# Optimization experiments

Measured on AMD Instinct MI355X. Metric: run time of the kernel, lower is better.

Reference implementation:

```python
import jax, jax.numpy as jnp
import numpy as np

B, C, H, W = 4, 256, 64, 64
G, K, P = 4, 7, 3          # groups, kernel size, padding
RED = 32                   # out_channels // reduce_ratio
BN_EPS = 1e-5


def setup_inputs() -> dict:
    key = jax.random.key(0)
    ks = jax.random.split(key, 3)
    x = jax.random.normal(ks[0], (B, C, H, W), dtype=jnp.float32)
    w_reduce = jax.random.normal(ks[1], (RED, C), dtype=jnp.float32) * (1.0 / np.sqrt(C))
    bn_gamma = jnp.ones((RED,), dtype=jnp.float32)
    bn_beta = jnp.zeros((RED,), dtype=jnp.float32)
    w_span = jax.random.normal(ks[2], (K * K * G, RED), dtype=jnp.float32) * (1.0 / np.sqrt(RED))
    b_span = jnp.zeros((K * K * G,), dtype=jnp.float32)
    return {"x": x, "w_reduce": w_reduce, "bn_gamma": bn_gamma,
            "bn_beta": bn_beta, "w_span": w_span, "b_span": b_span}


def _involution(x, w_reduce, bn_gamma, bn_beta, w_span, b_span):
    # ---- dynamic kernel generation (stride=1 so AvgPool is identity) ----
    red = jnp.einsum('oc,bchw->bohw', w_reduce, x)                 # [B,RED,H,W]
    # BatchNorm2d forward with batch statistics (training-mode math)
    mean = red.mean(axis=(0, 2, 3), keepdims=True)
    var = red.var(axis=(0, 2, 3), keepdims=True)
    red_n = (red - mean) * jax.lax.rsqrt(var + BN_EPS)
    act = jax.nn.relu(red_n * bn_gamma[None, :, None, None] + bn_beta[None, :, None, None])
    ker = jnp.einsum('oc,bchw->bohw', w_span, act) + b_span[None, :, None, None]
    ker = ker.reshape(B, G, K * K, H, W)                           # [B,G,KK,H,W]

    # ---- unfold: K*K shifted views of the padded input ----
    xp = jnp.pad(x, ((0, 0), (0, 0), (P, P), (P, P)))
    patches = jnp.stack([xp[:, :, i:i + H, j:j + W]
                         for i in range(K) for j in range(K)], axis=2)  # [B,C,KK,H,W]
    patches = patches.reshape(B, G, C // G, K * K, H, W)

    # ---- per-pixel weighted neighborhood sum ----
    out = jnp.einsum('bgkhw,bgckhw->bgchw', ker, patches)
    return out.reshape(B, C, H, W)


def reference(x, w_reduce, bn_gamma, bn_beta, w_span, b_span):
    return _involution(x, w_reduce, bn_gamma, bn_beta, w_span, b_span)
```

## Files before the change

### kernel.cpp

```cpp
#include <hip/hip_runtime.h>

#define B_ 4
#define C_ 256
#define H_ 64
#define W_ 64
#define HW_ 4096
#define K_ 7
#define P_ 3
#define KK_ 49
#define KKG_ 196
#define RED_ 32
#define NSTAT_ 16384.0f
#define BN_EPS_ 1e-5f
#define OCH_ 28

#define CPB_ 8
#define TH_ 16
#define TRS_ 22
#define TRW_ 76

__global__ __launch_bounds__(256) void k_reduce(const float* __restrict__ x,
                                               const float* __restrict__ wr,
                                               float4* __restrict__ part,
                                               float* __restrict__ gstats) {
    const int tid = threadIdx.x;
    const int og  = blockIdx.y;
    const int bz  = blockIdx.z;
    if (blockIdx.x == 0 && og == 0 && bz == 0 && tid < 64) gstats[tid] = 0.0f;

    const int p2 = blockIdx.x * 256 + tid;
    const int b  = p2 >> 11;
    const int hw = (p2 & 2047) << 1;
    const float* xp = x + ((size_t)(b * C_ + bz * 64)) * HW_ + hw;
    const float* wp = wr + (og * 8) * C_ + bz * 64;

    float a[8][2];
#pragma unroll
    for (int oi = 0; oi < 8; ++oi) { a[oi][0] = 0.f; a[oi][1] = 0.f; }
#pragma unroll 8
    for (int cc = 0; cc < 64; ++cc) {
        const float2 v = *(const float2*)(xp + (size_t)cc * HW_);
#pragma unroll
        for (int oi = 0; oi < 8; ++oi) {
            const float wv = wp[oi * C_ + cc];
            a[oi][0] = fmaf(wv, v.x, a[oi][0]);
            a[oi][1] = fmaf(wv, v.y, a[oi][1]);
        }
    }
    const int slot = bz * 4 + og;
    float4* pp0 = part + (((size_t)(slot * 2 + 0)) << 14) + (p2 << 1);
    float4* pp1 = part + (((size_t)(slot * 2 + 1)) << 14) + (p2 << 1);
    pp0[0] = make_float4(a[0][0], a[1][0], a[2][0], a[3][0]);
    pp0[1] = make_float4(a[0][1], a[1][1], a[2][1], a[3][1]);
    pp1[0] = make_float4(a[4][0], a[5][0], a[6][0], a[7][0]);
    pp1[1] = make_float4(a[4][1], a[5][1], a[6][1], a[7][1]);
}

__global__ __launch_bounds__(256) void k_comb(const float4* __restrict__ part,
                                              float4* __restrict__ red,
                                              float* __restrict__ gsum,
                                              float* __restrict__ gsq) {
    __shared__ float lsum[4][8];
    const int tid  = threadIdx.x;
    const int lane = tid & 63;
    const int wv   = tid >> 6;
    const int oq   = blockIdx.y;
    const int og   = oq >> 1;
    const int half = oq & 1;
    const int p    = blockIdx.x * 256 + tid;

    float4 s = make_float4(0.f, 0.f, 0.f, 0.f);
#pragma unroll
    for (int bz = 0; bz < 4; ++bz) {
        const float4 v = part[(((size_t)((bz * 4 + og) * 2 + half)) << 14) + p];
        s.x += v.x; s.y += v.y; s.z += v.z; s.w += v.w;
    }
    red[((size_t)oq << 14) + p] = s;

    float s0 = s.x, s1 = s.y, s2 = s.z, s3 = s.w;
    float q0 = s.x*s.x, q1 = s.y*s.y, q2 = s.z*s.z, q3 = s.w*s.w;
#pragma unroll
    for (int off = 32; off > 0; off >>= 1) {
        s0 += __shfl_down(s0, off);  q0 += __shfl_down(q0, off);
        s1 += __shfl_down(s1, off);  q1 += __shfl_down(q1, off);
        s2 += __shfl_down(s2, off);  q2 += __shfl_down(q2, off);
        s3 += __shfl_down(s3, off);  q3 += __shfl_down(q3, off);
    }
    if (lane == 0) {
        lsum[wv][0] = s0; lsum[wv][1] = s1; lsum[wv][2] = s2; lsum[wv][3] = s3;
        lsum[wv][4] = q0; lsum[wv][5] = q1; lsum[wv][6] = q2; lsum[wv][7] = q3;
    }
    __syncthreads();
    if (tid < 8) {
        const float v = lsum[0][tid] + lsum[1][tid] + lsum[2][tid] + lsum[3][tid];
        float* dst = (tid < 4) ? &gsum[oq * 4 + tid] : &gsq[oq * 4 + (tid - 4)];
        atomicAdd(dst, v);
    }
}

__global__ __launch_bounds__(256) void k_span(const float4* __restrict__ red,
                                              const float* __restrict__ wspan,
                                              const float* __restrict__ bspan,
                                              const float* __restrict__ gsum,
                                              const float* __restrict__ gsq,
                                              const float* __restrict__ gamma,
                                              const float* __restrict__ beta,
                                              float* __restrict__ ker) {
    __shared__ float sc_l[RED_], sh_l[RED_];
    const int tid   = threadIdx.x;
    const int chunk = blockIdx.y;
    const int obase = chunk * OCH_;
    if (tid < RED_) {
        const float m   = gsum[tid] * (1.0f / NSTAT_);
        const float var = gsq[tid] * (1.0f / NSTAT_) - m * m;
        const float inv = rsqrtf(var + BN_EPS_);
        const float sc  = gamma[tid] * inv;
        sc_l[tid] = sc;
        sh_l[tid] = beta[tid] - m * sc;
    }
    __syncthreads();

    const int p  = blockIdx.x * 256 + tid;
    const int b  = p >> 12;
    const int hw = p & 4095;

    float act[RED_];
#pragma unroll
    for (int og = 0; og < 8; ++og) {
        const float4 v = red[((size_t)og << 14) + p];
        act[4*og+0] = v.x; act[4*og+1] = v.y; act[4*og+2] = v.z; act[4*og+3] = v.w;
    }
#pragma unroll
    for (int o = 0; o < RED_; ++o)
        act[o] = fmaxf(fmaf(act[o], sc_l[o], sh_l[o]), 0.0f);

    float* kp = ker + ((size_t)b * KKG_ + obase) * HW_ + hw;
    const float* wp = wspan + (size_t)obase * RED_;
#pragma unroll 4
    for (int o = 0; o < OCH_; ++o) {
        float s = bspan[obase + o];
#pragma unroll
        for (int c = 0; c < RED_; ++c)
            s = fmaf(wp[o * RED_ + c], act[c], s);
        kp[(size_t)o * HW_] = s;
    }
}

__global__ __launch_bounds__(256) void k_inv(const float* __restrict__ x,
                                             const float* __restrict__ ker,
                                             float* __restrict__ out) {
    __shared__ float tile[CPB_][TRS_][TRW_];
    const int tid = threadIdx.x;
    const int wg  = tid & 7;
    const int hq  = (tid >> 3) & 15;
    const int cq  = tid >> 7;
    const int bx  = blockIdx.x;
    const int ht  = bx & 3;
    const int cblk = (bx >> 2) & 31;
    const int b   = bx >> 7;
    const int h0  = ht << 4;
    const int c0  = cblk << 3;
    const int g   = c0 >> 6;
    const int w0  = wg << 3;
    const int h   = h0 + hq;

    const float4 fz = make_float4(0.f, 0.f, 0.f, 0.f);
#pragma unroll
    for (int it = 0; it < 11; ++it) {
        const int i   = it * 256 + tid;
        const int ci  = i / (TRS_ * 16);
        const int rem = i - ci * (TRS_ * 16);
        const int r   = rem >> 4;
        const int seg = rem & 15;
        const int hh  = h0 + r - P_;
        float4 v = fz;
        if (hh >= 0 && hh < H_)
            v = *(const float4*)(x + (((size_t)(b * C_ + c0 + ci)) << 12) + (hh << 6) + (seg << 2));
        *(float4*)&tile[ci][r][4 + (seg << 2)] = v;
    }
    for (int i = tid; i < CPB_ * TRS_ * 2; i += 256) {
        const int ci  = i / (TRS_ * 2);
        const int rem = i - ci * (TRS_ * 2);
        const int r   = rem >> 1;
        *(float4*)&tile[ci][r][(rem & 1) ? 68 : 0] = fz;
    }
    __syncthreads();

    const int cA = cq << 2;
    const float* kp = ker + (((size_t)b * KKG_ + g * KK_) << 12) + (h << 6) + w0;

    float acc[4][8];
#pragma unroll
    for (int c = 0; c < 4; ++c)
#pragma unroll
        for (int dw = 0; dw < 8; ++dw) acc[c][dw] = 0.f;

#pragma unroll
    for (int i = 0; i < K_; ++i) {
        const int r = hq + i;
        float win[4][16];
#pragma unroll
        for (int c = 0; c < 4; ++c) {
            const float* t = &tile[cA + c][r][w0];
#pragma unroll
            for (int s = 0; s < 4; ++s) {
                const float4 v = *(const float4*)(t + (s << 2));
                win[c][4*s+0]=v.x; win[c][4*s+1]=v.y; win[c][4*s+2]=v.z; win[c][4*s+3]=v.w;
            }
        }
#pragma unroll
        for (int j = 0; j < K_; ++j) {
            const float* kpp = kp + ((size_t)(i * K_ + j) << 12);
            const float4 k0 = *(const float4*)kpp;
            const float4 k1 = *(const float4*)(kpp + 4);
            const float kv[8] = {k0.x, k0.y, k0.z, k0.w, k1.x, k1.y, k1.z, k1.w};
#pragma unroll
            for (int c = 0; c < 4; ++c)
#pragma unroll
                for (int dw = 0; dw < 8; ++dw)
                    acc[c][dw] = fmaf(kv[dw], win[c][dw + j + 1], acc[c][dw]);
        }
    }

#pragma unroll
    for (int c = 0; c < 4; ++c) {
        float* o = out + (((size_t)(b * C_ + c0 + cA + c)) << 12) + (h << 6) + w0;
        *(float4*)(o)     = make_float4(acc[c][0], acc[c][1], acc[c][2], acc[c][3]);
        *(float4*)(o + 4) = make_float4(acc[c][4], acc[c][5], acc[c][6], acc[c][7]);
    }
}

extern "C" void kernel_launch(void* const* d_in, const int* in_sizes, int n_in,
                              void* d_out, int out_size, void* d_ws, size_t ws_size,
                              hipStream_t stream) {
    const float* x     = (const float*)d_in[0];
    const float* wr    = (const float*)d_in[1];
    const float* gamma = (const float*)d_in[2];
    const float* beta  = (const float*)d_in[3];
    const float* wspan = (const float*)d_in[4];
    const float* bspan = (const float*)d_in[5];
    float* out = (float*)d_out;
    float* ws  = (float*)d_ws;

    float*  redf  = ws;
    float*  gsum  = ws + 524288;
    float*  gsq   = gsum + 32;
    float*  ker   = ws + 524416;
    float*  partf = ws + 524416 + 3211264;
    float4* red   = (float4*)redf;
    float4* part  = (float4*)partf;

    hipLaunchKernelGGL(k_reduce, dim3(32, 4, 4), dim3(256), 0, stream, x, wr, part, gsum);
    hipLaunchKernelGGL(k_comb,   dim3(64, 8),    dim3(256), 0, stream, part, red, gsum, gsq);
    hipLaunchKernelGGL(k_span,   dim3(64, 7),    dim3(256), 0, stream, red, wspan, bspan, gsum, gsq, gamma, beta, ker);
    hipLaunchKernelGGL(k_inv,    dim3(512),      dim3(256), 0, stream, x, ker, out);
}
```

Before: 58.72 us.

## Compute all 32 reduce channels per thread and regroup involution blocks by group

k_reduce now has each thread produce all 32 reduced outputs for one pixel, instead of 8 outputs for two pixels split across four output-group blocks. Each x value is therefore loaded once per channel slice rather than four times, cutting redundant global reads. The cost is more accumulator registers and fewer blocks (256 instead of 512), which may lower occupancy. k_inv block indexing is also remapped so that consecutive blocks share a group's kernel weights, which should improve cache locality for the ker reads.

```diff
diff --git a/kernel.cpp b/kernel.cpp
--- a/kernel.cpp
+++ b/kernel.cpp
@@ -24,36 +24,31 @@
                                                float4* __restrict__ part,
                                                float* __restrict__ gstats) {
     const int tid = threadIdx.x;
-    const int og  = blockIdx.y;
-    const int bz  = blockIdx.z;
-    if (blockIdx.x == 0 && og == 0 && bz == 0 && tid < 64) gstats[tid] = 0.0f;
-
-    const int p2 = blockIdx.x * 256 + tid;
-    const int b  = p2 >> 11;
-    const int hw = (p2 & 2047) << 1;
+    const int bz  = blockIdx.y;
+    if (blockIdx.x == 0 && bz == 0 && tid < 64) gstats[tid] = 0.0f;
+
+    const int p  = blockIdx.x * 256 + tid;
+    const int b  = p >> 12;
+    const int hw = p & 4095;
     const float* xp = x + ((size_t)(b * C_ + bz * 64)) * HW_ + hw;
-    const float* wp = wr + (og * 8) * C_ + bz * 64;
-
-    float a[8][2];
-#pragma unroll
-    for (int oi = 0; oi < 8; ++oi) { a[oi][0] = 0.f; a[oi][1] = 0.f; }
+    const float* wp = wr + bz * 64;
+
+    float a[32];
+#pragma unroll
+    for (int o = 0; o < 32; ++o) a[o] = 0.0f;
+
 #pragma unroll 8
     for (int cc = 0; cc < 64; ++cc) {
-        const float2 v = *(const float2*)(xp + (size_t)cc * HW_);
-#pragma unroll
-        for (int oi = 0; oi < 8; ++oi) {
-            const float wv = wp[oi * C_ + cc];
-            a[oi][0] = fmaf(wv, v.x, a[oi][0]);
-            a[oi][1] = fmaf(wv, v.y, a[oi][1]);
-        }
-    }
-    const int slot = bz * 4 + og;
-    float4* pp0 = part + (((size_t)(slot * 2 + 0)) << 14) + (p2 << 1);
-    float4* pp1 = part + (((size_t)(slot * 2 + 1)) << 14) + (p2 << 1);
-    pp0[0] = make_float4(a[0][0], a[1][0], a[2][0], a[3][0]);
-    pp0[1] = make_float4(a[0][1], a[1][1], a[2][1], a[3][1]);
-    pp1[0] = make_float4(a[4][0], a[5][0], a[6][0], a[7][0]);
-    pp1[1] = make_float4(a[4][1], a[5][1], a[6][1], a[7][1]);
+        const float v = xp[(size_t)cc * HW_];
+#pragma unroll
+        for (int o = 0; o < 32; ++o)
+            a[o] = fmaf(wp[o * C_ + cc], v, a[o]);
+    }
+
+#pragma unroll
+    for (int q = 0; q < 8; ++q)
+        part[(((size_t)(bz * 8 + q)) << 14) + p] =
+            make_float4(a[4*q], a[4*q+1], a[4*q+2], a[4*q+3]);
 }
 
 __global__ __launch_bounds__(256) void k_comb(const float4* __restrict__ part,
@@ -65,14 +60,12 @@
     const int lane = tid & 63;
     const int wv   = tid >> 6;
     const int oq   = blockIdx.y;
-    const int og   = oq >> 1;
-    const int half = oq & 1;
     const int p    = blockIdx.x * 256 + tid;
 
     float4 s = make_float4(0.f, 0.f, 0.f, 0.f);
 #pragma unroll
     for (int bz = 0; bz < 4; ++bz) {
-        const float4 v = part[(((size_t)((bz * 4 + og) * 2 + half)) << 14) + p];
+        const float4 v = part[(((size_t)(bz * 8 + oq)) << 14) + p];
         s.x += v.x; s.y += v.y; s.z += v.z; s.w += v.w;
     }
     red[((size_t)oq << 14) + p] = s;
@@ -155,12 +148,14 @@
     const int hq  = (tid >> 3) & 15;
     const int cq  = tid >> 7;
     const int bx  = blockIdx.x;
-    const int ht  = bx & 3;
-    const int cblk = (bx >> 2) & 31;
-    const int b   = bx >> 7;
+    const int gid = bx & 63;
+    const int m   = bx >> 6;
+    const int b   = gid >> 4;
+    const int g   = (gid >> 2) & 3;
+    const int ht  = gid & 3;
+    const int cblk = (g << 3) + m;
     const int h0  = ht << 4;
     const int c0  = cblk << 3;
-    const int g   = c0 >> 6;
     const int w0  = wg << 3;
     const int h   = h0 + hq;
 
@@ -250,8 +245,8 @@
     float4* red   = (float4*)redf;
     float4* part  = (float4*)partf;
 
-    hipLaunchKernelGGL(k_reduce, dim3(32, 4, 4), dim3(256), 0, stream, x, wr, part, gsum);
-    hipLaunchKernelGGL(k_comb,   dim3(64, 8),    dim3(256), 0, stream, part, red, gsum, gsq);
-    hipLaunchKernelGGL(k_span,   dim3(64, 7),    dim3(256), 0, stream, red, wspan, bspan, gsum, gsq, gamma, beta, ker);
-    hipLaunchKernelGGL(k_inv,    dim3(512),      dim3(256), 0, stream, x, ker, out);
-}
+    hipLaunchKernelGGL(k_reduce, dim3(64, 4),   dim3(256), 0, stream, x, wr, part, gsum);
+    hipLaunchKernelGGL(k_comb,   dim3(64, 8),   dim3(256), 0, stream, part, red, gsum, gsq);
+    hipLaunchKernelGGL(k_span,   dim3(64, 7),   dim3(256), 0, stream, red, wspan, bspan, gsum, gsq, gamma, beta, ker);
+    hipLaunchKernelGGL(k_inv,    dim3(512),     dim3(256), 0, stream, x, ker, out);
+}
```

Result: slower. 78.84 us (+34.3%).
